# Kernel tuning notes

Hardware: AMD Instinct MI355X
Metric: run time of the kernel (lower is better)

Reference implementation:

```python
import jax, jax.numpy as jnp
import numpy as np

D_MODEL = 2048
N_HEADS = 16
HEAD_DIM = D_MODEL // N_HEADS  # 128
ROPE_THETA = 10000.0
BATCH = 2
SEQ_LEN = 2048  # == window_size -> dense causal SDPA path


def setup_inputs() -> dict:
    key = jax.random.key(0)
    ks = jax.random.split(key, 5)
    scale = 1.0 / np.sqrt(D_MODEL)
    x = jax.random.normal(ks[0], (BATCH, SEQ_LEN, D_MODEL), dtype=jnp.float32)
    # torch nn.Linear weights are stored (out_features, in_features); y = x @ W.T
    Wq = jax.random.normal(ks[1], (D_MODEL, D_MODEL), dtype=jnp.float32) * scale
    Wk = jax.random.normal(ks[2], (D_MODEL, D_MODEL), dtype=jnp.float32) * scale
    Wv = jax.random.normal(ks[3], (D_MODEL, D_MODEL), dtype=jnp.float32) * scale
    Wo = jax.random.normal(ks[4], (D_MODEL, D_MODEL), dtype=jnp.float32) * scale
    return {"x": x, "Wq": Wq, "Wk": Wk, "Wv": Wv, "Wo": Wo}


def _apply_rope(x):
    # x: [B, H, S, HEAD_DIM]; interleaved-pair RoPE, positions 0..S-1
    S = x.shape[2]
    inv_freq = 1.0 / (ROPE_THETA ** (jnp.arange(0, HEAD_DIM, 2, dtype=jnp.float32) / HEAD_DIM))
    t = jnp.arange(S, dtype=jnp.float32)
    freqs = jnp.outer(t, inv_freq)            # [S, HEAD_DIM//2]
    cos = jnp.cos(freqs)
    sin = jnp.sin(freqs)
    x1 = x[..., 0::2]
    x2 = x[..., 1::2]
    rot = jnp.stack([x1 * cos - x2 * sin, x1 * sin + x2 * cos], axis=-1)  # [B,H,S,hd/2,2]
    return rot.reshape(x.shape)


def reference(x, Wq, Wk, Wv, Wo):
    B, S, _ = x.shape
    q = (x @ Wq.T).reshape(B, S, N_HEADS, HEAD_DIM).transpose(0, 2, 1, 3)  # [B,H,S,D]
    k = (x @ Wk.T).reshape(B, S, N_HEADS, HEAD_DIM).transpose(0, 2, 1, 3)
    v = (x @ Wv.T).reshape(B, S, N_HEADS, HEAD_DIM).transpose(0, 2, 1, 3)
    q = _apply_rope(q)
    k = _apply_rope(k)
    scores = jnp.einsum("bhqd,bhkd->bhqk", q, k) / np.sqrt(HEAD_DIM).astype(np.float32)
    causal = jnp.tril(jnp.ones((S, S), dtype=bool))
    scores = jnp.where(causal, scores, -jnp.inf)
    attn = jax.nn.softmax(scores, axis=-1)
    out = jnp.einsum("bhqk,bhkd->bhqd", attn, v)
    out = out.transpose(0, 2, 1, 3).reshape(B, S, N_HEADS * HEAD_DIM)
    return out @ Wo.T
```

## Files before the change

### kernel.cpp

```cpp
#include <hip/hip_runtime.h>
#include <stdint.h>

#define D_MODEL 2048
#define SEQ     2048
#define BATCH   2
#define NHEAD   16
#define HD      128
#define MROWS   (BATCH*SEQ)

typedef short short8 __attribute__((ext_vector_type(8)));
typedef float f32x4  __attribute__((ext_vector_type(4)));

__device__ __forceinline__ unsigned short f2b(float f) {
  unsigned int u = __float_as_uint(f);
  u += 0x7fffu + ((u >> 16) & 1u);
  return (unsigned short)(u >> 16);
}
__device__ __forceinline__ float b2f(unsigned short s) {
  return __uint_as_float(((unsigned int)s) << 16);
}
__device__ __forceinline__ void gll16(const void* g, void* l) {
  __builtin_amdgcn_global_load_lds((const __attribute__((address_space(1))) void*)g,
                                   (__attribute__((address_space(3))) void*)l, 16, 0, 0);
}

__global__ __launch_bounds__(256) void cast_all(
    const float* __restrict__ x,  const float* __restrict__ Wq,
    const float* __restrict__ Wk, const float* __restrict__ Wv,
    const float* __restrict__ Wo, unsigned short* __restrict__ dst)
{
  size_t e = ((size_t)blockIdx.x * 256 + threadIdx.x) * 4;
  const size_t XN = (size_t)MROWS * D_MODEL;
  const size_t WN = (size_t)D_MODEL * D_MODEL;
  const float* src; size_t off;
  if (e < XN) { src = x; off = e; }
  else {
    size_t e2 = e - XN;
    int w = (int)(e2 >> 22);
    off = e2 & (WN - 1);
    src = (w == 0) ? Wq : (w == 1) ? Wk : (w == 2) ? Wv : Wo;
  }
  float4 v = *(const float4*)(src + off);
  ushort4 o;
  o.x = f2b(v.x); o.y = f2b(v.y); o.z = f2b(v.z); o.w = f2b(v.w);
  *(ushort4*)(dst + e) = o;
}

__device__ __forceinline__ void gemm_core(
    const unsigned short* __restrict__ A, const unsigned short* __restrict__ Bw,
    unsigned short* As, unsigned short* Bs, int m0, int n0, int tid,
    f32x4 (&acc)[4][4])
{
  const int K = D_MODEL;
  const int wave = tid >> 6, lane = tid & 63, l15 = lane & 15, quad = lane >> 4;
  const int wr = wave >> 1, wc = wave & 1;

  for (int kt = 0; kt < K; kt += 32) {
    #pragma unroll
    for (int c = 0; c < 2; ++c) {
      int chunk = c * 256 + tid;
      const unsigned short* ga = A  + (size_t)(m0 + (chunk >> 2)) * K + kt + (chunk & 3) * 8;
      const unsigned short* gb = Bw + (size_t)(n0 + (chunk >> 2)) * K + kt + (chunk & 3) * 8;
      gll16(ga, As + (size_t)(c * 256 + wave * 64) * 8);
      gll16(gb, Bs + (size_t)(c * 256 + wave * 64) * 8);
    }
    __syncthreads();
    short8 af[4], bfr[4];
    #pragma unroll
    for (int mi = 0; mi < 4; ++mi)
      af[mi] = *(const short8*)(As + (wr * 64 + mi * 16 + l15) * 32 + quad * 8);
    #pragma unroll
    for (int ni = 0; ni < 4; ++ni)
      bfr[ni] = *(const short8*)(Bs + (wc * 64 + ni * 16 + l15) * 32 + quad * 8);
    #pragma unroll
    for (int mi = 0; mi < 4; ++mi)
      #pragma unroll
      for (int ni = 0; ni < 4; ++ni)
        acc[mi][ni] = __builtin_amdgcn_mfma_f32_16x16x32_bf16(af[mi], bfr[ni], acc[mi][ni], 0, 0, 0);
    __syncthreads();
  }
}

__global__ __launch_bounds__(256) void gemm_qkv(
    const unsigned short* __restrict__ Axb,
    const unsigned short* __restrict__ Wq, const unsigned short* __restrict__ Wk,
    const unsigned short* __restrict__ Wv,
    unsigned short* __restrict__ Qh, unsigned short* __restrict__ Kh,
    unsigned short* __restrict__ Vt)
{
  __shared__ unsigned short As[128 * 32], Bs[128 * 32];
  const int z = blockIdx.z;
  const unsigned short* Bw = (z == 0) ? Wq : (z == 1) ? Wk : Wv;
  const int m0 = blockIdx.y * 128, n0 = blockIdx.x * 128;
  f32x4 acc[4][4];
  #pragma unroll
  for (int i = 0; i < 4; ++i)
    #pragma unroll
    for (int j = 0; j < 4; ++j) acc[i][j] = (f32x4){0.f, 0.f, 0.f, 0.f};
  gemm_core(Axb, Bw, As, Bs, m0, n0, threadIdx.x, acc);

  const int tid = threadIdx.x, wave = tid >> 6, lane = tid & 63;
  const int l15 = lane & 15, quad = lane >> 4, wr = wave >> 1, wc = wave & 1;
  if (z < 2) {
    unsigned short* dst = z ? Kh : Qh;
    #pragma unroll
    for (int mi = 0; mi < 4; ++mi)
      #pragma unroll
      for (int ni = 0; ni < 4; ++ni) {
        int row0 = m0 + wr * 64 + mi * 16 + quad * 4;
        int col  = n0 + wc * 64 + ni * 16 + l15;
        int h = col >> 7, d = col & (HD - 1);
        #pragma unroll
        for (int r = 0; r < 4; ++r) {
          int m = row0 + r; int bb = m >> 11; int s = m & (SEQ - 1);
          dst[((size_t)(bb * NHEAD + h) * SEQ + s) * HD + d] = f2b(acc[mi][ni][r]);
        }
      }
  } else {
    #pragma unroll
    for (int mi = 0; mi < 4; ++mi)
      #pragma unroll
      for (int ni = 0; ni < 4; ++ni) {
        int row0 = m0 + wr * 64 + mi * 16 + quad * 4;
        int col  = n0 + wc * 64 + ni * 16 + l15;
        int h = col >> 7, d = col & (HD - 1);
        int bb = row0 >> 11; int s = row0 & (SEQ - 1);
        ushort4 pk;
        pk.x = f2b(acc[mi][ni][0]); pk.y = f2b(acc[mi][ni][1]);
        pk.z = f2b(acc[mi][ni][2]); pk.w = f2b(acc[mi][ni][3]);
        *(ushort4*)(Vt + ((size_t)(bb * NHEAD + h) * HD + d) * SEQ + s) = pk;
      }
  }
}

__global__ __launch_bounds__(256) void gemm_out(
    const unsigned short* __restrict__ A, const unsigned short* __restrict__ Wo,
    float* __restrict__ C)
{
  __shared__ unsigned short As[128 * 32], Bs[128 * 32];
  const int m0 = blockIdx.y * 128, n0 = blockIdx.x * 128;
  f32x4 acc[4][4];
  #pragma unroll
  for (int i = 0; i < 4; ++i)
    #pragma unroll
    for (int j = 0; j < 4; ++j) acc[i][j] = (f32x4){0.f, 0.f, 0.f, 0.f};
  gemm_core(A, Wo, As, Bs, m0, n0, threadIdx.x, acc);

  const int tid = threadIdx.x, wave = tid >> 6, lane = tid & 63;
  const int l15 = lane & 15, quad = lane >> 4, wr = wave >> 1, wc = wave & 1;
  #pragma unroll
  for (int mi = 0; mi < 4; ++mi)
    #pragma unroll
    for (int ni = 0; ni < 4; ++ni) {
      int row0 = m0 + wr * 64 + mi * 16 + quad * 4;
      int col  = n0 + wc * 64 + ni * 16 + l15;
      #pragma unroll
      for (int r = 0; r < 4; ++r)
        C[(size_t)(row0 + r) * D_MODEL + col] = acc[mi][ni][r];
    }
}

__global__ __launch_bounds__(256) void rope_k(unsigned short* __restrict__ Qh,
                                              unsigned short* __restrict__ Kh)
{
  unsigned short* P = blockIdx.y ? Kh : Qh;
  int rid = blockIdx.x * 4 + (threadIdx.x >> 6);
  int i = threadIdx.x & 63;
  int s = rid & (SEQ - 1);
  size_t base = (size_t)rid * HD + 2 * i;
  float inv = exp2f(-(float)i * (13.287712379549449f / 64.0f));
  float ang = (float)s * inv;
  float sn, cs; sincosf(ang, &sn, &cs);
  unsigned int pk = *(const unsigned int*)(P + base);
  float x1 = b2f((unsigned short)(pk & 0xffffu));
  float x2 = b2f((unsigned short)(pk >> 16));
  unsigned short o0 = f2b(x1 * cs - x2 * sn);
  unsigned short o1 = f2b(x1 * sn + x2 * cs);
  *(unsigned int*)(P + base) = (unsigned int)o0 | ((unsigned int)o1 << 16);
}

__global__ __launch_bounds__(256) void attn_k(
    const unsigned short* __restrict__ Qh, const unsigned short* __restrict__ Kh,
    const unsigned short* __restrict__ Vt, unsigned short* __restrict__ Aout)
{
  __shared__ unsigned short Ks[64 * 128];
  __shared__ unsigned short Vs[128 * 64];
  __shared__ unsigned short sPb[4][16 * 72];
  const int tid = threadIdx.x;
  const int wave = tid >> 6, lane = tid & 63, l15 = lane & 15, quad = lane >> 4;
  const int bh = blockIdx.y;
  const int b = bh >> 4, h = bh & 15;
  const unsigned short* Qb = Qh + (size_t)bh * SEQ * HD;
  const unsigned short* Kb = Kh + (size_t)bh * SEQ * HD;
  const unsigned short* Vb = Vt + (size_t)bh * HD * SEQ;
  unsigned short* pw = &sPb[wave][0];
  const float scl = 0.08838834764831845f * 1.4426950408889634f;

  #pragma unroll
  for (int half = 0; half < 2; ++half) {
    const int tile = half ? (31 - blockIdx.x) : blockIdx.x;
    const int q0b = tile * 64;
    const int q0w = q0b + wave * 16;
    const int q = q0w + l15;

    short8 qf[4];
    #pragma unroll
    for (int c = 0; c < 4; ++c)
      qf[c] = *(const short8*)(Qb + (size_t)(q0w + l15) * HD + c * 32 + quad * 8);

    f32x4 o[8];
    #pragma unroll
    for (int dj = 0; dj < 8; ++dj) o[dj] = (f32x4){0.f, 0.f, 0.f, 0.f};
    float ms = -1e30f, ls = 0.f;

    const int trips = tile + 1;
    for (int it = 0; it < trips; ++it) {
      const int k0 = it * 64;
      __syncthreads();
      #pragma unroll
      for (int c = 0; c < 4; ++c) {
        int slot = c * 256 + tid;
        int kr = slot >> 4, pch = slot & 15;
        gll16(Kb + (size_t)(k0 + kr) * HD + ((pch ^ (kr & 15)) * 8), Ks + slot * 8);
      }
      #pragma unroll
      for (int c = 0; c < 4; ++c) {
        int slot = c * 256 + tid;
        int vr = slot >> 3, pch = slot & 7;
        gll16(Vb + (size_t)vr * SEQ + k0 + ((pch ^ (vr & 7)) * 8), Vs + slot * 8);
      }
      __syncthreads();

      f32x4 st[4];
      #pragma unroll
      for (int ni = 0; ni < 4; ++ni) st[ni] = (f32x4){0.f, 0.f, 0.f, 0.f};
      #pragma unroll
      for (int ni = 0; ni < 4; ++ni) {
        const int rowb = (ni * 16 + l15) * 128;
        #pragma unroll
        for (int c = 0; c < 4; ++c) {
          short8 kf = *(const short8*)(Ks + rowb + (((c * 4 + quad) ^ l15) * 8));
          st[ni] = __builtin_amdgcn_mfma_f32_16x16x32_bf16(kf, qf[c], st[ni], 0, 0, 0);
        }
      }

      if (k0 + 63 > q0w) {
        #pragma unroll
        for (int ni = 0; ni < 4; ++ni)
          #pragma unroll
          for (int r = 0; r < 4; ++r) {
            int k = k0 + ni * 16 + quad * 4 + r;
            if (k > q) st[ni][r] = -1e30f;
          }
      }

      float lm = -1e30f;
      #pragma unroll
      for (int ni = 0; ni < 4; ++ni)
        #pragma unroll
        for (int r = 0; r < 4; ++r) lm = fmaxf(lm, st[ni][r]);
      lm = fmaxf(lm, __shfl_xor(lm, 16, 64));
      lm = fmaxf(lm, __shfl_xor(lm, 32, 64));
      float mn = fmaxf(ms, lm);
      float al = exp2f((ms - mn) * scl);
      ms = mn;
      float nm = mn * scl;
      float rs = 0.f;
      #pragma unroll
      for (int ni = 0; ni < 4; ++ni)
        #pragma unroll
        for (int r = 0; r < 4; ++r) {
          float p = exp2f(fmaf(st[ni][r], scl, -nm));
          st[ni][r] = p;
          rs += p;
        }
      rs += __shfl_xor(rs, 16, 64);
      rs += __shfl_xor(rs, 32, 64);
      ls = ls * al + rs;
      #pragma unroll
      for (int dj = 0; dj < 8; ++dj) o[dj] *= al;

      #pragma unroll
      for (int ni = 0; ni < 4; ++ni) {
        ushort4 pk;
        pk.x = f2b(st[ni][0]); pk.y = f2b(st[ni][1]);
        pk.z = f2b(st[ni][2]); pk.w = f2b(st[ni][3]);
        *(ushort4*)(pw + l15 * 72 + ni * 16 + quad * 4) = pk;
      }
      short8 pf0 = *(const short8*)(pw + l15 * 72 + quad * 8);
      short8 pf1 = *(const short8*)(pw + l15 * 72 + 32 + quad * 8);

      #pragma unroll
      for (int dj = 0; dj < 8; ++dj) {
        const int vrow = (dj * 16 + l15) * 64;
        short8 v0 = *(const short8*)(Vs + vrow + (((quad) ^ (l15 & 7)) * 8));
        short8 v1 = *(const short8*)(Vs + vrow + (((4 + quad) ^ (l15 & 7)) * 8));
        o[dj] = __builtin_amdgcn_mfma_f32_16x16x32_bf16(v0, pf0, o[dj], 0, 0, 0);
        o[dj] = __builtin_amdgcn_mfma_f32_16x16x32_bf16(v1, pf1, o[dj], 0, 0, 0);
      }
    }

    float rl = 1.0f / ls;
    #pragma unroll
    for (int dj = 0; dj < 8; ++dj) {
      ushort4 pk;
      pk.x = f2b(o[dj][0] * rl); pk.y = f2b(o[dj][1] * rl);
      pk.z = f2b(o[dj][2] * rl); pk.w = f2b(o[dj][3] * rl);
      *(ushort4*)(Aout + ((size_t)(b * SEQ + q)) * D_MODEL + h * HD + dj * 16 + quad * 4) = pk;
    }
  }
}

extern "C" void kernel_launch(void* const* d_in, const int* in_sizes, int n_in,
                              void* d_out, int out_size, void* d_ws, size_t ws_size,
                              hipStream_t stream)
{
  const float* x  = (const float*)d_in[0];
  const float* Wq = (const float*)d_in[1];
  const float* Wk = (const float*)d_in[2];
  const float* Wv = (const float*)d_in[3];
  const float* Wo = (const float*)d_in[4];
  float* out = (float*)d_out;

  unsigned short* xb  = (unsigned short*)d_ws;
  unsigned short* wqb = xb  + 8388608;
  unsigned short* wkb = wqb + 4194304;
  unsigned short* wvb = wkb + 4194304;
  unsigned short* wob = wvb + 4194304;
  unsigned short* qh  = wob + 4194304;
  unsigned short* kh  = qh  + 8388608;
  unsigned short* vt  = kh  + 8388608;
  unsigned short* ao  = vt  + 8388608;

  cast_all<<<24576, 256, 0, stream>>>(x, Wq, Wk, Wv, Wo, xb);
  gemm_qkv<<<dim3(16, 32, 3), 256, 0, stream>>>(xb, wqb, wkb, wvb, qh, kh, vt);
  rope_k<<<dim3(16384, 2), 256, 0, stream>>>(qh, kh);
  attn_k<<<dim3(16, 32), 256, 0, stream>>>(qh, kh, vt, ao);
  gemm_out<<<dim3(16, 32), 256, 0, stream>>>(ao, wob, out);
}
```

Before: 429.5 us.

## Rewrite projection GEMMs with double-buffered swizzled LDS pipeline and larger tiles

Replaces the single-buffered 128x128 K=32 GEMM core with a templated double-buffered pipeline (K=64 stages, async global-to-LDS loads, explicit vmcnt waits, XOR-swizzled LDS layout, setprio around MFMA bursts). QKV projection becomes one fused 256x256-tile GEMM over the concatenated weight buffer using 512-thread blocks, and the output GEMM uses 128x256 tiles. The goal is to hide global load latency, avoid LDS bank conflicts and raise reuse per load. The trade-offs are higher LDS and register pressure, plus reliance on Wq/Wk/Wv being contiguous in the workspace.

```diff
diff --git a/kernel.cpp b/kernel.cpp
--- a/kernel.cpp
+++ b/kernel.cpp
@@ -22,6 +22,11 @@
 __device__ __forceinline__ void gll16(const void* g, void* l) {
   __builtin_amdgcn_global_load_lds((const __attribute__((address_space(1))) void*)g,
                                    (__attribute__((address_space(3))) void*)l, 16, 0, 0);
+}
+__device__ __forceinline__ void barrier_nodrain() {
+  asm volatile("" ::: "memory");
+  __builtin_amdgcn_s_barrier();
+  asm volatile("" ::: "memory");
 }
 
 __global__ __launch_bounds__(256) void cast_all(
@@ -46,69 +51,149 @@
   *(ushort4*)(dst + e) = o;
 }
 
-__device__ __forceinline__ void gemm_core(
+template<int BM, int BN>
+__device__ __forceinline__ void gemm_pipe(
     const unsigned short* __restrict__ A, const unsigned short* __restrict__ Bw,
-    unsigned short* As, unsigned short* Bs, int m0, int n0, int tid,
-    f32x4 (&acc)[4][4])
-{
-  const int K = D_MODEL;
+    unsigned short* __restrict__ As, unsigned short* __restrict__ Bs,
+    int m0, int n0, int tid, f32x4 (&acc)[BM / 32][4])
+{
+  constexpr int K  = D_MODEL;
+  constexpr int NT = K / 64;
+  constexpr int LA = BM / 64, LB = BN / 64;
+  constexpr int LT = LA + LB;
+  constexpr int MI = BM / 32, MH = MI / 2;
   const int wave = tid >> 6, lane = tid & 63, l15 = lane & 15, quad = lane >> 4;
-  const int wr = wave >> 1, wc = wave & 1;
-
-  for (int kt = 0; kt < K; kt += 32) {
-    #pragma unroll
-    for (int c = 0; c < 2; ++c) {
-      int chunk = c * 256 + tid;
-      const unsigned short* ga = A  + (size_t)(m0 + (chunk >> 2)) * K + kt + (chunk & 3) * 8;
-      const unsigned short* gb = Bw + (size_t)(n0 + (chunk >> 2)) * K + kt + (chunk & 3) * 8;
-      gll16(ga, As + (size_t)(c * 256 + wave * 64) * 8);
-      gll16(gb, Bs + (size_t)(c * 256 + wave * 64) * 8);
-    }
-    __syncthreads();
-    short8 af[4], bfr[4];
-    #pragma unroll
-    for (int mi = 0; mi < 4; ++mi)
-      af[mi] = *(const short8*)(As + (wr * 64 + mi * 16 + l15) * 32 + quad * 8);
-    #pragma unroll
-    for (int ni = 0; ni < 4; ++ni)
-      bfr[ni] = *(const short8*)(Bs + (wc * 64 + ni * 16 + l15) * 32 + quad * 8);
-    #pragma unroll
-    for (int mi = 0; mi < 4; ++mi)
-      #pragma unroll
-      for (int ni = 0; ni < 4; ++ni)
-        acc[mi][ni] = __builtin_amdgcn_mfma_f32_16x16x32_bf16(af[mi], bfr[ni], acc[mi][ni], 0, 0, 0);
-    __syncthreads();
+  const int wr = wave >> 2, wc = wave & 3;
+  const int sw = l15 & 7;
+  const int arow = wr * (BM / 2) + l15;
+  const int brow = wc * (BN / 4) + l15;
+
+  auto stage = [&](int buf, int t) {
+    const int kt = t * 64;
+    #pragma unroll
+    for (int i = 0; i < LA; ++i) {
+      int slot = i * 512 + tid;
+      int row = slot >> 3, ch = slot & 7;
+      gll16(A + (size_t)(m0 + row) * K + kt + ((ch ^ (row & 7)) * 8),
+            As + (size_t)buf * (BM * 64) + (size_t)(i * 512 + wave * 64) * 8);
+    }
+    #pragma unroll
+    for (int i = 0; i < LB; ++i) {
+      int slot = i * 512 + tid;
+      int row = slot >> 3, ch = slot & 7;
+      gll16(Bw + (size_t)(n0 + row) * K + kt + ((ch ^ (row & 7)) * 8),
+            Bs + (size_t)buf * (BN * 64) + (size_t)(i * 512 + wave * 64) * 8);
+    }
+  };
+
+  stage(0, 0);
+  stage(1, 1);
+
+  short8 ah[MH][2], bf[4][2];
+
+  #pragma unroll 1
+  for (int t = 0; t < NT; ++t) {
+    const int cur = t & 1;
+    if (t < NT - 1) {
+      if constexpr (LT == 8) asm volatile("s_waitcnt vmcnt(8)" ::: "memory");
+      else                   asm volatile("s_waitcnt vmcnt(6)" ::: "memory");
+    } else {
+      asm volatile("s_waitcnt vmcnt(0)" ::: "memory");
+    }
+    barrier_nodrain();
+
+    const unsigned short* as = As + cur * (BM * 64);
+    const unsigned short* bs = Bs + cur * (BN * 64);
+
+    #pragma unroll
+    for (int mi = 0; mi < MH; ++mi)
+      #pragma unroll
+      for (int ks = 0; ks < 2; ++ks)
+        ah[mi][ks] = *(const short8*)(as + (arow + mi * 16) * 64 + (((ks * 4 + quad) ^ sw) * 8));
+    #pragma unroll
+    for (int ni = 0; ni < 2; ++ni)
+      #pragma unroll
+      for (int ks = 0; ks < 2; ++ks)
+        bf[ni][ks] = *(const short8*)(bs + (brow + ni * 16) * 64 + (((ks * 4 + quad) ^ sw) * 8));
+    __builtin_amdgcn_s_setprio(1);
+    #pragma unroll
+    for (int mi = 0; mi < MH; ++mi)
+      #pragma unroll
+      for (int ni = 0; ni < 2; ++ni)
+        #pragma unroll
+        for (int ks = 0; ks < 2; ++ks)
+          acc[mi][ni] = __builtin_amdgcn_mfma_f32_16x16x32_bf16(ah[mi][ks], bf[ni][ks], acc[mi][ni], 0, 0, 0);
+    __builtin_amdgcn_s_setprio(0);
+
+    #pragma unroll
+    for (int ni = 2; ni < 4; ++ni)
+      #pragma unroll
+      for (int ks = 0; ks < 2; ++ks)
+        bf[ni][ks] = *(const short8*)(bs + (brow + ni * 16) * 64 + (((ks * 4 + quad) ^ sw) * 8));
+    __builtin_amdgcn_s_setprio(1);
+    #pragma unroll
+    for (int mi = 0; mi < MH; ++mi)
+      #pragma unroll
+      for (int ni = 2; ni < 4; ++ni)
+        #pragma unroll
+        for (int ks = 0; ks < 2; ++ks)
+          acc[mi][ni] = __builtin_amdgcn_mfma_f32_16x16x32_bf16(ah[mi][ks], bf[ni][ks], acc[mi][ni], 0, 0, 0);
+    __builtin_amdgcn_s_setprio(0);
+
+    #pragma unroll
+    for (int mi = 0; mi < MH; ++mi)
+      #pragma unroll
+      for (int ks = 0; ks < 2; ++ks)
+        ah[mi][ks] = *(const short8*)(as + (arow + (mi + MH) * 16) * 64 + (((ks * 4 + quad) ^ sw) * 8));
+    __builtin_amdgcn_s_setprio(1);
+    #pragma unroll
+    for (int mi = 0; mi < MH; ++mi)
+      #pragma unroll
+      for (int ni = 2; ni < 4; ++ni)
+        #pragma unroll
+        for (int ks = 0; ks < 2; ++ks)
+          acc[mi + MH][ni] = __builtin_amdgcn_mfma_f32_16x16x32_bf16(ah[mi][ks], bf[ni][ks], acc[mi + MH][ni], 0, 0, 0);
+    #pragma unroll
+    for (int mi = 0; mi < MH; ++mi)
+      #pragma unroll
+      for (int ni = 0; ni < 2; ++ni)
+        #pragma unroll
+        for (int ks = 0; ks < 2; ++ks)
+          acc[mi + MH][ni] = __builtin_amdgcn_mfma_f32_16x16x32_bf16(ah[mi][ks], bf[ni][ks], acc[mi + MH][ni], 0, 0, 0);
+    __builtin_amdgcn_s_setprio(0);
+
+    barrier_nodrain();
+    if (t + 2 < NT) stage(cur, t + 2);
   }
 }
 
-__global__ __launch_bounds__(256) void gemm_qkv(
-    const unsigned short* __restrict__ Axb,
-    const unsigned short* __restrict__ Wq, const unsigned short* __restrict__ Wk,
-    const unsigned short* __restrict__ Wv,
+__global__ __launch_bounds__(512, 2) void gemm_qkv2(
+    const unsigned short* __restrict__ Axb, const unsigned short* __restrict__ Wqkv,
     unsigned short* __restrict__ Qh, unsigned short* __restrict__ Kh,
     unsigned short* __restrict__ Vt)
 {
-  __shared__ unsigned short As[128 * 32], Bs[128 * 32];
-  const int z = blockIdx.z;
-  const unsigned short* Bw = (z == 0) ? Wq : (z == 1) ? Wk : Wv;
-  const int m0 = blockIdx.y * 128, n0 = blockIdx.x * 128;
-  f32x4 acc[4][4];
+  __shared__ unsigned short As[2 * 256 * 64];
+  __shared__ unsigned short Bs[2 * 256 * 64];
+  const int m0 = blockIdx.y * 256, n0g = blockIdx.x * 256;
+  f32x4 acc[8][4];
   #pragma unroll
-  for (int i = 0; i < 4; ++i)
+  for (int i = 0; i < 8; ++i)
     #pragma unroll
     for (int j = 0; j < 4; ++j) acc[i][j] = (f32x4){0.f, 0.f, 0.f, 0.f};
-  gemm_core(Axb, Bw, As, Bs, m0, n0, threadIdx.x, acc);
+
+  gemm_pipe<256, 256>(Axb, Wqkv, As, Bs, m0, n0g, threadIdx.x, acc);
 
   const int tid = threadIdx.x, wave = tid >> 6, lane = tid & 63;
-  const int l15 = lane & 15, quad = lane >> 4, wr = wave >> 1, wc = wave & 1;
+  const int l15 = lane & 15, quad = lane >> 4, wr = wave >> 2, wc = wave & 3;
+  const int z = n0g >> 11;
   if (z < 2) {
     unsigned short* dst = z ? Kh : Qh;
     #pragma unroll
-    for (int mi = 0; mi < 4; ++mi)
+    for (int mi = 0; mi < 8; ++mi)
       #pragma unroll
       for (int ni = 0; ni < 4; ++ni) {
-        int row0 = m0 + wr * 64 + mi * 16 + quad * 4;
-        int col  = n0 + wc * 64 + ni * 16 + l15;
+        int row0 = m0 + wr * 128 + mi * 16 + quad * 4;
+        int col  = (n0g + wc * 64 + ni * 16 + l15) & (D_MODEL - 1);
         int h = col >> 7, d = col & (HD - 1);
         #pragma unroll
         for (int r = 0; r < 4; ++r) {
@@ -118,11 +203,11 @@
       }
   } else {
     #pragma unroll
-    for (int mi = 0; mi < 4; ++mi)
+    for (int mi = 0; mi < 8; ++mi)
       #pragma unroll
       for (int ni = 0; ni < 4; ++ni) {
-        int row0 = m0 + wr * 64 + mi * 16 + quad * 4;
-        int col  = n0 + wc * 64 + ni * 16 + l15;
+        int row0 = m0 + wr * 128 + mi * 16 + quad * 4;
+        int col  = (n0g + wc * 64 + ni * 16 + l15) & (D_MODEL - 1);
         int h = col >> 7, d = col & (HD - 1);
         int bb = row0 >> 11; int s = row0 & (SEQ - 1);
         ushort4 pk;
@@ -133,21 +218,23 @@
   }
 }
 
-__global__ __launch_bounds__(256) void gemm_out(
+__global__ __launch_bounds__(512, 2) void gemm_out2(
     const unsigned short* __restrict__ A, const unsigned short* __restrict__ Wo,
     float* __restrict__ C)
 {
-  __shared__ unsigned short As[128 * 32], Bs[128 * 32];
-  const int m0 = blockIdx.y * 128, n0 = blockIdx.x * 128;
+  __shared__ unsigned short As[2 * 128 * 64];
+  __shared__ unsigned short Bs[2 * 256 * 64];
+  const int m0 = blockIdx.y * 128, n0 = blockIdx.x * 256;
   f32x4 acc[4][4];
   #pragma unroll
   for (int i = 0; i < 4; ++i)
     #pragma unroll
     for (int j = 0; j < 4; ++j) acc[i][j] = (f32x4){0.f, 0.f, 0.f, 0.f};
-  gemm_core(A, Wo, As, Bs, m0, n0, threadIdx.x, acc);
+
+  gemm_pipe<128, 256>(A, Wo, As, Bs, m0, n0, threadIdx.x, acc);
 
   const int tid = threadIdx.x, wave = tid >> 6, lane = tid & 63;
-  const int l15 = lane & 15, quad = lane >> 4, wr = wave >> 1, wc = wave & 1;
+  const int l15 = lane & 15, quad = lane >> 4, wr = wave >> 2, wc = wave & 3;
   #pragma unroll
   for (int mi = 0; mi < 4; ++mi)
     #pragma unroll
@@ -332,9 +419,10 @@
   unsigned short* vt  = kh  + 8388608;
   unsigned short* ao  = vt  + 8388608;
 
+  (void)wkb; (void)wvb;
   cast_all<<<24576, 256, 0, stream>>>(x, Wq, Wk, Wv, Wo, xb);
-  gemm_qkv<<<dim3(16, 32, 3), 256, 0, stream>>>(xb, wqb, wkb, wvb, qh, kh, vt);
+  gemm_qkv2<<<dim3(24, 16), 512, 0, stream>>>(xb, wqb, qh, kh, vt);
   rope_k<<<dim3(16384, 2), 256, 0, stream>>>(qh, kh);
   attn_k<<<dim3(16, 32), 256, 0, stream>>>(qh, kh, vt, ao);
-  gemm_out<<<dim3(16, 32), 256, 0, stream>>>(ao, wob, out);
-}
+  gemm_out2<<<dim3(8, 32), 512, 0, stream>>>(ao, wob, out);
+}
```

After: 418.1 us. -2.7%, faster.
